# Kernel optimization log

Measured on AMD Instinct MI355X. Metric: run time of the kernel, lower is better.

## Reference

```python
import jax, jax.numpy as jnp
import numpy as np

K_MASK = -2.3819763e38  # gemma masking constant


def apply_rope(inputs, positions, head_dim):
    # inputs: [B, T, N, H], positions: [B, T]
    half = head_dim // 2
    fraction = 2.0 * jnp.arange(half, dtype=jnp.float32) / head_dim
    timescale = 10000.0 ** fraction                      # [half]
    sinusoid = positions[..., None].astype(jnp.float32) / timescale  # [B, T, half]
    sin = jnp.sin(sinusoid)[:, :, None, :]               # [B, T, 1, half]
    cos = jnp.cos(sinusoid)[:, :, None, :]
    first, second = jnp.split(inputs, 2, axis=-1)
    out = jnp.concatenate([first * cos - second * sin,
                           second * cos + first * sin], axis=-1)
    return out.astype(inputs.dtype)


def setup_inputs() -> dict:
    key = jax.random.key(0)
    k0, k1, k2, k3 = jax.random.split(key, 4)
    B, T, D, N, H = 4, 1024, 2048, 16, 128
    x = jax.random.normal(k0, (B, T, D), dtype=jnp.float32)
    wq = jax.random.normal(k1, (N, D, H), dtype=jnp.float32) * 0.02
    wkv = jax.random.normal(k2, (2, 1, D, H), dtype=jnp.float32) * 0.02  # MQA: 1 kv head
    wo = jax.random.normal(k3, (N, H, D), dtype=jnp.float32) * 0.02
    segment_pos = jnp.broadcast_to(jnp.arange(T, dtype=jnp.int32), (B, T))
    attn_mask = jnp.broadcast_to(jnp.tril(jnp.ones((T, T), dtype=bool)), (B, T, T))
    return {"x": x, "wq": wq, "wkv": wkv, "wo": wo,
            "segment_pos": segment_pos, "attn_mask": attn_mask}


def reference(x, wq, wkv, wo, segment_pos, attn_mask):
    N, _, H = wq.shape
    # projections
    q = jnp.einsum('BTD,NDH->BTNH', x, wq)          # [B,T,N,H]
    kv = jnp.einsum('BSD,CKDH->CBSKH', x, wkv)      # [2,B,S,1,H]
    k, v = kv[0], kv[1]
    # RoPE + scaling
    q = apply_rope(q, segment_pos, H) * (H ** -0.5)
    k = apply_rope(k, segment_pos, H)
    # MQA head repeat: 1 kv head -> N heads
    k = jnp.repeat(k, N, axis=-2)                   # [B,S,N,H]
    v = jnp.repeat(v, N, axis=-2)
    # attention with manual masked softmax
    logits = jnp.einsum('BTNH,BSNH->BTNS', q, k)
    padded = jnp.where(attn_mask[:, :, None, :], logits, K_MASK)
    probs = jax.nn.softmax(padded, axis=-1).astype(k.dtype)
    encoded = jnp.einsum('BTNS,BSNH->BTNH', probs, v)
    return jnp.einsum('BTNH,NHD->BTD', encoded, wo)
```

## Files before the change

### kernel.cpp

```cpp
#include <hip/hip_runtime.h>
#include <cstdint>
#include <cstddef>

typedef unsigned short u16;
typedef __attribute__((ext_vector_type(8))) short bf16x8;
typedef __attribute__((ext_vector_type(4))) float f32x4;
typedef __attribute__((ext_vector_type(16))) float f32x16;
typedef __attribute__((ext_vector_type(4))) uint32_t u32x4;

#define B_ 4
#define T_ 1024
#define D_ 2048
#define N_ 16
#define H_ 128
#define BT_ (B_ * T_)
#define KMASK (-2.3819763e38f)

__device__ __forceinline__ u16 f2bf(float f) {
  uint32_t u = __builtin_bit_cast(uint32_t, f);
  u += 0x7FFFu + ((u >> 16) & 1u);
  return (u16)(u >> 16);
}
__device__ __forceinline__ float bf2f(uint32_t u) {
  return __builtin_bit_cast(float, u << 16);
}

__device__ __forceinline__ float xhalf_max(float x) {
  return fmaxf(x, __shfl_xor(x, 32, 64));
}
__device__ __forceinline__ float xhalf_add(float x) {
  return x + __shfl_xor(x, 32, 64);
}

__device__ __forceinline__ void gload16(const void* g, void* l) {
  __builtin_amdgcn_global_load_lds((const __attribute__((address_space(1))) void*)g,
                                   (__attribute__((address_space(3))) void*)l, 16, 0, 0);
}

__global__ __launch_bounds__(256) void convert_x_kernel(const float* __restrict__ x,
                                                        u16* __restrict__ xb) {
  int i = (blockIdx.x * 256 + threadIdx.x) * 8;
  float4 v0 = *(const float4*)(x + i);
  float4 v1 = *(const float4*)(x + i + 4);
  uint4 o;
  o.x = (uint32_t)f2bf(v0.x) | ((uint32_t)f2bf(v0.y) << 16);
  o.y = (uint32_t)f2bf(v0.z) | ((uint32_t)f2bf(v0.w) << 16);
  o.z = (uint32_t)f2bf(v1.x) | ((uint32_t)f2bf(v1.y) << 16);
  o.w = (uint32_t)f2bf(v1.z) | ((uint32_t)f2bf(v1.w) << 16);
  *(uint4*)(xb + i) = o;
}

__global__ __launch_bounds__(256) void transpose_kernel(const float* __restrict__ src,
                                                        u16* __restrict__ dst, int R, int C) {
  __shared__ float tile[32][33];
  const int z = blockIdx.z;
  const float* s = src + (size_t)z * R * C;
  u16* d = dst + (size_t)z * R * C;
  const int tx = threadIdx.x, ty = threadIdx.y;
  const int r0 = blockIdx.y * 32, c0 = blockIdx.x * 32;
#pragma unroll
  for (int i = 0; i < 4; ++i)
    tile[ty + i * 8][tx] = s[(size_t)(r0 + ty + i * 8) * C + (c0 + tx)];
  __syncthreads();
#pragma unroll
  for (int i = 0; i < 4; ++i)
    d[(size_t)(c0 + ty + i * 8) * R + (r0 + tx)] = f2bf(tile[tx][ty + i * 8]);
}

__global__ __launch_bounds__(256) void rope_table_kernel(float* __restrict__ costab,
                                                         float* __restrict__ sintab) {
  int idx = blockIdx.x * 256 + threadIdx.x;
  int p = idx >> 6, i = idx & 63;
  float ts = powf(10000.0f, (float)i * (1.0f / 64.0f));
  float ang = (float)p / ts;
  costab[idx] = cosf(ang);
  sintab[idx] = sinf(ang);
}

__global__ __launch_bounds__(256) void proj_gemm_kernel(
    const u16* __restrict__ xb, const u16* __restrict__ wqT, const u16* __restrict__ wkvT,
    u16* __restrict__ qraw, u16* __restrict__ kraw, u16* __restrict__ vT) {
  __shared__ alignas(16) u16 a_lds[128 * 64];
  __shared__ alignas(16) u16 b_lds[128 * 64];
  const int bid = blockIdx.x;
  const int newbid = (bid & 7) * 72 + (bid >> 3);
  const int y = newbid >> 5;
  const int m0 = (newbid & 31) * 128;
  const u16* Bt = (y < N_) ? (wqT + (size_t)y * H_ * D_) : (wkvT + (size_t)(y - N_) * H_ * D_);
  const int tid = threadIdx.x;
  const int w = tid >> 6, lane = tid & 63;
  const int g = lane >> 4, li = lane & 15;
  const int mrow = (w >> 1) * 64, wc = (w & 1) * 64;
  f32x4 acc[4][4];
#pragma unroll
  for (int i = 0; i < 4; ++i)
#pragma unroll
    for (int j = 0; j < 4; ++j) acc[i][j] = (f32x4){0.f, 0.f, 0.f, 0.f};

  for (int k0 = 0; k0 < D_; k0 += 64) {
    __syncthreads();
#pragma unroll
    for (int it = 0; it < 4; ++it) {
      int chunk = it * 256 + tid;
      int row = chunk >> 3, cu = chunk & 7;
      gload16(xb + (size_t)(m0 + row) * D_ + k0 + ((cu ^ (row & 7)) << 3), &a_lds[chunk * 8]);
    }
#pragma unroll
    for (int it = 0; it < 4; ++it) {
      int chunk = it * 256 + tid;
      int row = chunk >> 3, cu = chunk & 7;
      gload16(Bt + (size_t)row * D_ + k0 + ((cu ^ (row & 7)) << 3), &b_lds[chunk * 8]);
    }
    __syncthreads();
#pragma unroll
    for (int c2 = 0; c2 < 2; ++c2) {
      bf16x8 af[4], bfr[4];
#pragma unroll
      for (int i = 0; i < 4; ++i) {
        int row = mrow + i * 16 + li;
        af[i] = *(const bf16x8*)((const char*)a_lds +
                                 row * 128 + ((c2 * 64 + g * 16) ^ ((row & 7) << 4)));
      }
#pragma unroll
      for (int j = 0; j < 4; ++j) {
        int row = wc + j * 16 + li;
        bfr[j] = *(const bf16x8*)((const char*)b_lds +
                                  row * 128 + ((c2 * 64 + g * 16) ^ ((row & 7) << 4)));
      }
#pragma unroll
      for (int i = 0; i < 4; ++i)
#pragma unroll
        for (int j = 0; j < 4; ++j)
          acc[i][j] = __builtin_amdgcn_mfma_f32_16x16x32_bf16(af[i], bfr[j], acc[i][j], 0, 0, 0);
    }
  }

  const int b = m0 >> 10;
  if (y == N_ + 1) {
    const int tbase0 = (m0 & 1023) + mrow;
#pragma unroll
    for (int i = 0; i < 4; ++i) {
      int tbase = tbase0 + i * 16 + g * 4;
#pragma unroll
      for (int j = 0; j < 4; ++j) {
        int h = wc + j * 16 + li;
        ushort4 pk;
        pk.x = f2bf(acc[i][j][0]);
        pk.y = f2bf(acc[i][j][1]);
        pk.z = f2bf(acc[i][j][2]);
        pk.w = f2bf(acc[i][j][3]);
        *(ushort4*)(vT + ((size_t)(b * H_ + h)) * T_ + tbase) = pk;
      }
    }
  } else {
    size_t rowbase = (y < N_) ? ((size_t)(b * N_ + y) * T_ + (m0 & 1023)) : (size_t)m0;
    u16* dst0 = (y < N_) ? qraw : kraw;
#pragma unroll
    for (int i = 0; i < 4; ++i)
#pragma unroll
      for (int r = 0; r < 4; ++r) {
        int trow = mrow + i * 16 + g * 4 + r;
        u16* dst = dst0 + (rowbase + trow) * H_;
#pragma unroll
        for (int j = 0; j < 4; ++j) dst[wc + j * 16 + li] = f2bf(acc[i][j][r]);
      }
  }
}

__global__ __launch_bounds__(256) void rope_apply_k_kernel(
    const u16* __restrict__ kraw, const int* __restrict__ segment_pos,
    const float* __restrict__ costab, const float* __restrict__ sintab,
    u16* __restrict__ kb) {
  const int rid = blockIdx.x * 8 + (threadIdx.x >> 5);
  const int j = threadIdx.x & 31;
  const u16* src = kraw + (size_t)rid * H_;
  u16* dst = kb + (size_t)rid * H_;
  int p = segment_pos[rid];
  p = p < 0 ? 0 : (p > 1023 ? 1023 : p);
  uint32_t ua = *(const uint32_t*)(src + 2 * j);
  uint32_t ub = *(const uint32_t*)(src + 64 + 2 * j);
  float2 cv = *(const float2*)(costab + p * 64 + 2 * j);
  float2 sv = *(const float2*)(sintab + p * 64 + 2 * j);
  float f1a = bf2f(ua & 0xffffu), f1b = bf2f(ua >> 16);
  float f2a = bf2f(ub & 0xffffu), f2b = bf2f(ub >> 16);
  *(uint32_t*)(dst + 2 * j) =
      (uint32_t)f2bf(f1a * cv.x - f2a * sv.x) | ((uint32_t)f2bf(f1b * cv.y - f2b * sv.y) << 16);
  *(uint32_t*)(dst + 64 + 2 * j) =
      (uint32_t)f2bf(f2a * cv.x + f1a * sv.x) | ((uint32_t)f2bf(f2b * cv.y + f1b * sv.y) << 16);
}

__global__ __launch_bounds__(128) void attn_kernel(
    const u16* __restrict__ qraw, const u16* __restrict__ kb, const u16* __restrict__ vT,
    const int* __restrict__ segment_pos, const float* __restrict__ costab,
    const float* __restrict__ sintab, u16* __restrict__ enc) {
  __shared__ alignas(16) u16 k_lds[2][64 * 128];
  __shared__ alignas(16) u16 v_lds[128 * 64];
  const int bx = blockIdx.x;
  const int qt = 15 - (bx >> 6);
  const int bn = bx & 63;
  const int b = bn >> 4, n = bn & 15;
  const int tid = threadIdx.x, w = tid >> 6, lane = tid & 63;
  const int l31 = lane & 31, hi = lane >> 5;
  const int t = qt * 64 + w * 32 + l31;

  bf16x8 qf[8];
  {
    const u16* qrow = qraw + ((size_t)(b * N_ + n) * T_ + t) * H_;
#pragma unroll
    for (int kc = 0; kc < 8; ++kc) qf[kc] = *(const bf16x8*)(qrow + kc * 16 + hi * 8);
    int p = segment_pos[b * T_ + t];
    p = p < 0 ? 0 : (p > 1023 ? 1023 : p);
    const float scale = 0.12751743342f;
#pragma unroll
    for (int kc = 0; kc < 4; ++kc) {
      const float* cp = costab + p * 64 + kc * 16 + hi * 8;
      const float* sp = sintab + p * 64 + kc * 16 + hi * 8;
#pragma unroll
      for (int e = 0; e < 8; ++e) {
        float cv = cp[e], sv = sp[e];
        float f1 = bf2f((u16)qf[kc][e]);
        float f2 = bf2f((u16)qf[kc + 4][e]);
        qf[kc][e] = (short)f2bf((f1 * cv - f2 * sv) * scale);
        qf[kc + 4][e] = (short)f2bf((f2 * cv + f1 * sv) * scale);
      }
    }
  }

  f32x16 o[4];
#pragma unroll
  for (int hc = 0; hc < 4; ++hc)
#pragma unroll
    for (int r = 0; r < 16; ++r) o[hc][r] = 0.f;
  float m_ = -3e38f, lsum = 0.f;

  auto stageK = [&](int buf, int s0) {
#pragma unroll
    for (int it = 0; it < 8; ++it) {
      int chunk = it * 128 + tid;
      int row = chunk >> 4, cu = chunk & 15;
      gload16(kb + ((size_t)b * T_ + s0 + row) * H_ + ((cu ^ (row & 7)) << 3),
              &k_lds[buf][chunk * 8]);
    }
  };
  auto stageV = [&](int s0) {
#pragma unroll
    for (int it = 0; it < 8; ++it) {
      int chunk = it * 128 + tid;
      int row = chunk >> 3, cu = chunk & 7;
      gload16(vT + ((size_t)(b * H_ + row)) * T_ + s0 + ((cu ^ (row & 7)) << 3),
              &v_lds[chunk * 8]);
    }
  };

  const int nst = qt + 1;
  stageK(0, 0);
  int cur = 0;
  for (int st = 0; st < nst; ++st) {
    const int s0 = st * 64;
    const bool pre = (st + 1 < nst);
    stageV(s0);
    if (pre) stageK(cur ^ 1, s0 + 64);
    if (pre) asm volatile("s_waitcnt vmcnt(16)" ::: "memory");
    else     asm volatile("s_waitcnt vmcnt(8)" ::: "memory");
    __builtin_amdgcn_sched_barrier(0);
    __builtin_amdgcn_s_barrier();

    f32x16 sacc[2];
#pragma unroll
    for (int sub = 0; sub < 2; ++sub)
#pragma unroll
      for (int r = 0; r < 16; ++r) sacc[sub][r] = 0.f;
    __builtin_amdgcn_s_setprio(1);
#pragma unroll
    for (int kc = 0; kc < 8; ++kc)
#pragma unroll
      for (int sub = 0; sub < 2; ++sub) {
        int srow = sub * 32 + l31;
        bf16x8 kf = *(const bf16x8*)((const char*)&k_lds[cur][0] + srow * 256 +
                                     ((kc * 32 + hi * 16) ^ ((srow & 7) << 4)));
        sacc[sub] = __builtin_amdgcn_mfma_f32_32x32x16_bf16(kf, qf[kc], sacc[sub], 0, 0, 0);
      }
    __builtin_amdgcn_s_setprio(0);

    if (st == qt) {
#pragma unroll
      for (int sub = 0; sub < 2; ++sub)
#pragma unroll
        for (int r = 0; r < 16; ++r) {
          int s = s0 + sub * 32 + (r & 3) + 8 * (r >> 2) + 4 * hi;
          if (s > t) sacc[sub][r] = KMASK;
        }
    }

    float mx = -3e38f;
#pragma unroll
    for (int sub = 0; sub < 2; ++sub)
#pragma unroll
      for (int r = 0; r < 16; ++r) mx = fmaxf(mx, sacc[sub][r]);
    mx = xhalf_max(mx);
    if (__any(mx - m_ > 11.5f)) {
      float mn = fmaxf(m_, mx);
      float alpha = exp2f(m_ - mn);
      m_ = mn;
      lsum *= alpha;
#pragma unroll
      for (int hc = 0; hc < 4; ++hc)
#pragma unroll
        for (int r = 0; r < 16; ++r) o[hc][r] *= alpha;
    }
    float ps = 0.f;
#pragma unroll
    for (int sub = 0; sub < 2; ++sub)
#pragma unroll
      for (int r = 0; r < 16; ++r) {
        float pv = exp2f(sacc[sub][r] - m_);
        sacc[sub][r] = pv;
        ps += pv;
      }
    lsum += xhalf_add(ps);

    if (pre) asm volatile("s_waitcnt vmcnt(8)" ::: "memory");
    else     asm volatile("s_waitcnt vmcnt(0)" ::: "memory");
    __builtin_amdgcn_sched_barrier(0);
    __builtin_amdgcn_s_barrier();

    __builtin_amdgcn_s_setprio(1);
#pragma unroll
    for (int sc = 0; sc < 4; ++sc) {
      const int sub = sc >> 1, rb = (sc & 1) * 8;
      uint32_t a0, a1, b0, b1;
      asm("v_cvt_pk_bf16_f32 %0, %1, %2" : "=v"(a0) : "v"(sacc[sub][rb + 0]), "v"(sacc[sub][rb + 1]));
      asm("v_cvt_pk_bf16_f32 %0, %1, %2" : "=v"(a1) : "v"(sacc[sub][rb + 2]), "v"(sacc[sub][rb + 3]));
      asm("v_cvt_pk_bf16_f32 %0, %1, %2" : "=v"(b0) : "v"(sacc[sub][rb + 4]), "v"(sacc[sub][rb + 5]));
      asm("v_cvt_pk_bf16_f32 %0, %1, %2" : "=v"(b1) : "v"(sacc[sub][rb + 6]), "v"(sacc[sub][rb + 7]));
      uint32_t pa0 = (uint32_t)__shfl_xor((int)a0, 32, 64);
      uint32_t pa1 = (uint32_t)__shfl_xor((int)a1, 32, 64);
      uint32_t pb0 = (uint32_t)__shfl_xor((int)b0, 32, 64);
      uint32_t pb1 = (uint32_t)__shfl_xor((int)b1, 32, 64);
      uint32_t d0 = hi ? pb0 : a0;
      uint32_t d1 = hi ? pb1 : a1;
      uint32_t d2 = hi ? b0 : pa0;
      uint32_t d3 = hi ? b1 : pa1;
      u32x4 pdv = (u32x4){d0, d1, d2, d3};
      bf16x8 pf = __builtin_bit_cast(bf16x8, pdv);
#pragma unroll
      for (int hc = 0; hc < 4; ++hc) {
        int hrow = hc * 32 + l31;
        bf16x8 vf = *(const bf16x8*)((const char*)v_lds + hrow * 128 +
                                     ((sc * 32 + hi * 16) ^ ((hrow & 7) << 4)));
        o[hc] = __builtin_amdgcn_mfma_f32_32x32x16_bf16(vf, pf, o[hc], 0, 0, 0);
      }
    }
    __builtin_amdgcn_s_setprio(0);
    __builtin_amdgcn_s_barrier();
    cur ^= 1;
  }

  float inv = 1.0f / lsum;
  u16* dst = enc + ((size_t)(b * T_ + t)) * (N_ * H_) + n * H_;
#pragma unroll
  for (int hc = 0; hc < 4; ++hc)
#pragma unroll
    for (int rq = 0; rq < 4; ++rq) {
      ushort4 pk;
      pk.x = f2bf(o[hc][rq * 4 + 0] * inv);
      pk.y = f2bf(o[hc][rq * 4 + 1] * inv);
      pk.z = f2bf(o[hc][rq * 4 + 2] * inv);
      pk.w = f2bf(o[hc][rq * 4 + 3] * inv);
      *(ushort4*)(dst + hc * 32 + rq * 8 + hi * 4) = pk;
    }
}

__global__ __launch_bounds__(256) void out_gemm_kernel(const u16* __restrict__ enc,
                                                       const u16* __restrict__ woT,
                                                       float* __restrict__ out) {
  __shared__ alignas(16) u16 a_lds[128 * 64];
  __shared__ alignas(16) u16 b_lds[128 * 64];
  const int bid = blockIdx.x;
  const int newbid = (bid & 7) * 64 + (bid >> 3);
  const int m0 = (newbid & 31) * 128;
  const int n0 = (newbid >> 5) * 128;
  const int tid = threadIdx.x, w = tid >> 6, lane = tid & 63;
  const int g = lane >> 4, li = lane & 15;
  const int mrow = (w >> 1) * 64, wc = (w & 1) * 64;
  f32x4 acc[4][4];
#pragma unroll
  for (int i = 0; i < 4; ++i)
#pragma unroll
    for (int j = 0; j < 4; ++j) acc[i][j] = (f32x4){0.f, 0.f, 0.f, 0.f};

  for (int k0 = 0; k0 < D_; k0 += 64) {
    __syncthreads();
#pragma unroll
    for (int it = 0; it < 4; ++it) {
      int chunk = it * 256 + tid;
      int row = chunk >> 3, cu = chunk & 7;
      gload16(enc + (size_t)(m0 + row) * D_ + k0 + ((cu ^ (row & 7)) << 3), &a_lds[chunk * 8]);
    }
#pragma unroll
    for (int it = 0; it < 4; ++it) {
      int chunk = it * 256 + tid;
      int row = chunk >> 3, cu = chunk & 7;
      gload16(woT + (size_t)(n0 + row) * D_ + k0 + ((cu ^ (row & 7)) << 3), &b_lds[chunk * 8]);
    }
    __syncthreads();
#pragma unroll
    for (int c2 = 0; c2 < 2; ++c2) {
      bf16x8 af[4], bfr[4];
#pragma unroll
      for (int i = 0; i < 4; ++i) {
        int row = mrow + i * 16 + li;
        af[i] = *(const bf16x8*)((const char*)a_lds +
                                 row * 128 + ((c2 * 64 + g * 16) ^ ((row & 7) << 4)));
      }
#pragma unroll
      for (int j = 0; j < 4; ++j) {
        int row = wc + j * 16 + li;
        bfr[j] = *(const bf16x8*)((const char*)b_lds +
                                  row * 128 + ((c2 * 64 + g * 16) ^ ((row & 7) << 4)));
      }
#pragma unroll
      for (int i = 0; i < 4; ++i)
#pragma unroll
        for (int j = 0; j < 4; ++j)
          acc[i][j] = __builtin_amdgcn_mfma_f32_16x16x32_bf16(af[i], bfr[j], acc[i][j], 0, 0, 0);
    }
  }
#pragma unroll
  for (int i = 0; i < 4; ++i)
#pragma unroll
    for (int r = 0; r < 4; ++r) {
      int bt = m0 + mrow + i * 16 + g * 4 + r;
      float* dst = out + (size_t)bt * D_ + n0 + wc;
#pragma unroll
      for (int j = 0; j < 4; ++j) dst[j * 16 + li] = acc[i][j][r];
    }
}

extern "C" void kernel_launch(void* const* d_in, const int* in_sizes, int n_in,
                              void* d_out, int out_size, void* d_ws, size_t ws_size,
                              hipStream_t stream) {
  const float* x = (const float*)d_in[0];
  const float* wq = (const float*)d_in[1];
  const float* wkv = (const float*)d_in[2];
  const float* wo = (const float*)d_in[3];
  const int* segment_pos = (const int*)d_in[4];
  float* out = (float*)d_out;

  char* ws = (char*)d_ws;
  size_t off = 0;
  auto alloc = [&](size_t bytes) -> void* {
    void* p = ws + off;
    off += (bytes + 255) & ~(size_t)255;
    return p;
  };
  u16* xb   = (u16*)alloc((size_t)BT_ * D_ * 2);
  u16* wqT  = (u16*)alloc((size_t)N_ * H_ * D_ * 2);
  u16* wkvT = (u16*)alloc((size_t)2 * H_ * D_ * 2);
  u16* woT  = (u16*)alloc((size_t)D_ * N_ * H_ * 2);
  u16* qraw = (u16*)alloc((size_t)B_ * N_ * T_ * H_ * 2);
  u16* kb   = (u16*)alloc((size_t)B_ * T_ * H_ * 2);
  u16* kraw = (u16*)alloc((size_t)B_ * T_ * H_ * 2);
  u16* vT   = (u16*)alloc((size_t)B_ * H_ * T_ * 2);
  u16* enc  = (u16*)alloc((size_t)BT_ * N_ * H_ * 2);
  float* costab = (float*)alloc(1024 * 64 * 4);
  float* sintab = (float*)alloc(1024 * 64 * 4);

  convert_x_kernel<<<BT_ * D_ / 8 / 256, 256, 0, stream>>>(x, xb);
  dim3 tb(32, 8);
  transpose_kernel<<<dim3(H_ / 32, D_ / 32, N_), tb, 0, stream>>>(wq, wqT, D_, H_);
  transpose_kernel<<<dim3(H_ / 32, D_ / 32, 2), tb, 0, stream>>>(wkv, wkvT, D_, H_);
  transpose_kernel<<<dim3(D_ / 32, D_ / 32, 1), tb, 0, stream>>>(wo, woT, N_ * H_, D_);
  rope_table_kernel<<<256, 256, 0, stream>>>(costab, sintab);
  proj_gemm_kernel<<<576, 256, 0, stream>>>(xb, wqT, wkvT, qraw, kraw, vT);
  rope_apply_k_kernel<<<BT_ / 8, 256, 0, stream>>>(kraw, segment_pos, costab, sintab, kb);
  attn_kernel<<<1024, 128, 0, stream>>>(qraw, kb, vT, segment_pos, costab, sintab, enc);
  out_gemm_kernel<<<512, 256, 0, stream>>>(enc, woT, out);
}
```

Measured before the change: 180.2 us.

## Shrink attention blocks to single-wave 32-row tiles and drop block barriers

The attention kernel now runs one 64-lane wave per block over 32 query rows, with 32-key KV tiles, and launches twice as many blocks. With a single wave, the s_barrier calls are removed, and an lgkmcnt wait keeps LDS reads finished before the next staging overwrites the buffers. Smaller tiles give finer causal granularity, which means less wasted masked work on the diagonal, and more blocks for occupancy. The cost is that K/V tiles are no longer shared across two waves, so each K/V byte is loaded from global into LDS twice as often, and each step does fewer MFMAs per load.

```diff
diff --git a/kernel.cpp b/kernel.cpp
--- a/kernel.cpp
+++ b/kernel.cpp
@@ -189,19 +189,19 @@
       (uint32_t)f2bf(f2a * cv.x + f1a * sv.x) | ((uint32_t)f2bf(f2b * cv.y + f1b * sv.y) << 16);
 }
 
-__global__ __launch_bounds__(128) void attn_kernel(
+__global__ __launch_bounds__(64) void attn_kernel(
     const u16* __restrict__ qraw, const u16* __restrict__ kb, const u16* __restrict__ vT,
     const int* __restrict__ segment_pos, const float* __restrict__ costab,
     const float* __restrict__ sintab, u16* __restrict__ enc) {
-  __shared__ alignas(16) u16 k_lds[2][64 * 128];
-  __shared__ alignas(16) u16 v_lds[128 * 64];
+  __shared__ alignas(16) u16 k_lds[2][32 * 128];
+  __shared__ alignas(16) u16 v_lds[128 * 32];
   const int bx = blockIdx.x;
-  const int qt = 15 - (bx >> 6);
+  const int qt = 31 - (bx >> 6);
   const int bn = bx & 63;
   const int b = bn >> 4, n = bn & 15;
-  const int tid = threadIdx.x, w = tid >> 6, lane = tid & 63;
+  const int lane = threadIdx.x & 63;
   const int l31 = lane & 31, hi = lane >> 5;
-  const int t = qt * 64 + w * 32 + l31;
+  const int t = qt * 32 + l31;
 
   bf16x8 qf[8];
   {
@@ -236,7 +236,7 @@
   auto stageK = [&](int buf, int s0) {
 #pragma unroll
     for (int it = 0; it < 8; ++it) {
-      int chunk = it * 128 + tid;
+      int chunk = it * 64 + lane;
       int row = chunk >> 4, cu = chunk & 15;
       gload16(kb + ((size_t)b * T_ + s0 + row) * H_ + ((cu ^ (row & 7)) << 3),
               &k_lds[buf][chunk * 8]);
@@ -245,9 +245,9 @@
   auto stageV = [&](int s0) {
 #pragma unroll
     for (int it = 0; it < 8; ++it) {
-      int chunk = it * 128 + tid;
-      int row = chunk >> 3, cu = chunk & 7;
-      gload16(vT + ((size_t)(b * H_ + row)) * T_ + s0 + ((cu ^ (row & 7)) << 3),
+      int chunk = it * 64 + lane;
+      int row = chunk >> 2, cu = chunk & 3;
+      gload16(vT + ((size_t)(b * H_ + row)) * T_ + s0 + ((cu ^ (row & 3)) << 3),
               &v_lds[chunk * 8]);
     }
   };
@@ -256,47 +256,40 @@
   stageK(0, 0);
   int cur = 0;
   for (int st = 0; st < nst; ++st) {
-    const int s0 = st * 64;
+    const int s0 = st * 32;
     const bool pre = (st + 1 < nst);
+    asm volatile("s_waitcnt lgkmcnt(0)" ::: "memory");
+    __builtin_amdgcn_sched_barrier(0);
     stageV(s0);
-    if (pre) stageK(cur ^ 1, s0 + 64);
+    if (pre) stageK(cur ^ 1, s0 + 32);
     if (pre) asm volatile("s_waitcnt vmcnt(16)" ::: "memory");
     else     asm volatile("s_waitcnt vmcnt(8)" ::: "memory");
     __builtin_amdgcn_sched_barrier(0);
-    __builtin_amdgcn_s_barrier();
-
-    f32x16 sacc[2];
-#pragma unroll
-    for (int sub = 0; sub < 2; ++sub)
-#pragma unroll
-      for (int r = 0; r < 16; ++r) sacc[sub][r] = 0.f;
+
+    f32x16 sacc;
+#pragma unroll
+    for (int r = 0; r < 16; ++r) sacc[r] = 0.f;
     __builtin_amdgcn_s_setprio(1);
 #pragma unroll
-    for (int kc = 0; kc < 8; ++kc)
-#pragma unroll
-      for (int sub = 0; sub < 2; ++sub) {
-        int srow = sub * 32 + l31;
-        bf16x8 kf = *(const bf16x8*)((const char*)&k_lds[cur][0] + srow * 256 +
-                                     ((kc * 32 + hi * 16) ^ ((srow & 7) << 4)));
-        sacc[sub] = __builtin_amdgcn_mfma_f32_32x32x16_bf16(kf, qf[kc], sacc[sub], 0, 0, 0);
-      }
+    for (int kc = 0; kc < 8; ++kc) {
+      int srow = l31;
+      bf16x8 kf = *(const bf16x8*)((const char*)&k_lds[cur][0] + srow * 256 +
+                                   ((kc * 32 + hi * 16) ^ ((srow & 7) << 4)));
+      sacc = __builtin_amdgcn_mfma_f32_32x32x16_bf16(kf, qf[kc], sacc, 0, 0, 0);
+    }
     __builtin_amdgcn_s_setprio(0);
 
     if (st == qt) {
 #pragma unroll
-      for (int sub = 0; sub < 2; ++sub)
-#pragma unroll
-        for (int r = 0; r < 16; ++r) {
-          int s = s0 + sub * 32 + (r & 3) + 8 * (r >> 2) + 4 * hi;
-          if (s > t) sacc[sub][r] = KMASK;
-        }
+      for (int r = 0; r < 16; ++r) {
+        int s = s0 + (r & 3) + 8 * (r >> 2) + 4 * hi;
+        if (s > t) sacc[r] = KMASK;
+      }
     }
 
     float mx = -3e38f;
 #pragma unroll
-    for (int sub = 0; sub < 2; ++sub)
-#pragma unroll
-      for (int r = 0; r < 16; ++r) mx = fmaxf(mx, sacc[sub][r]);
+    for (int r = 0; r < 16; ++r) mx = fmaxf(mx, sacc[r]);
     mx = xhalf_max(mx);
     if (__any(mx - m_ > 11.5f)) {
       float mn = fmaxf(m_, mx);
@@ -310,29 +303,26 @@
     }
     float ps = 0.f;
 #pragma unroll
-    for (int sub = 0; sub < 2; ++sub)
-#pragma unroll
-      for (int r = 0; r < 16; ++r) {
-        float pv = exp2f(sacc[sub][r] - m_);
-        sacc[sub][r] = pv;
-        ps += pv;
-      }
+    for (int r = 0; r < 16; ++r) {
+      float pv = exp2f(sacc[r] - m_);
+      sacc[r] = pv;
+      ps += pv;
+    }
     lsum += xhalf_add(ps);
 
     if (pre) asm volatile("s_waitcnt vmcnt(8)" ::: "memory");
     else     asm volatile("s_waitcnt vmcnt(0)" ::: "memory");
     __builtin_amdgcn_sched_barrier(0);
-    __builtin_amdgcn_s_barrier();
 
     __builtin_amdgcn_s_setprio(1);
 #pragma unroll
-    for (int sc = 0; sc < 4; ++sc) {
-      const int sub = sc >> 1, rb = (sc & 1) * 8;
+    for (int sc = 0; sc < 2; ++sc) {
+      const int rb = sc * 8;
       uint32_t a0, a1, b0, b1;
-      asm("v_cvt_pk_bf16_f32 %0, %1, %2" : "=v"(a0) : "v"(sacc[sub][rb + 0]), "v"(sacc[sub][rb + 1]));
-      asm("v_cvt_pk_bf16_f32 %0, %1, %2" : "=v"(a1) : "v"(sacc[sub][rb + 2]), "v"(sacc[sub][rb + 3]));
-      asm("v_cvt_pk_bf16_f32 %0, %1, %2" : "=v"(b0) : "v"(sacc[sub][rb + 4]), "v"(sacc[sub][rb + 5]));
-      asm("v_cvt_pk_bf16_f32 %0, %1, %2" : "=v"(b1) : "v"(sacc[sub][rb + 6]), "v"(sacc[sub][rb + 7]));
+      asm("v_cvt_pk_bf16_f32 %0, %1, %2" : "=v"(a0) : "v"(sacc[rb + 0]), "v"(sacc[rb + 1]));
+      asm("v_cvt_pk_bf16_f32 %0, %1, %2" : "=v"(a1) : "v"(sacc[rb + 2]), "v"(sacc[rb + 3]));
+      asm("v_cvt_pk_bf16_f32 %0, %1, %2" : "=v"(b0) : "v"(sacc[rb + 4]), "v"(sacc[rb + 5]));
+      asm("v_cvt_pk_bf16_f32 %0, %1, %2" : "=v"(b1) : "v"(sacc[rb + 6]), "v"(sacc[rb + 7]));
       uint32_t pa0 = (uint32_t)__shfl_xor((int)a0, 32, 64);
       uint32_t pa1 = (uint32_t)__shfl_xor((int)a1, 32, 64);
       uint32_t pb0 = (uint32_t)__shfl_xor((int)b0, 32, 64);
@@ -346,13 +336,12 @@
 #pragma unroll
       for (int hc = 0; hc < 4; ++hc) {
         int hrow = hc * 32 + l31;
-        bf16x8 vf = *(const bf16x8*)((const char*)v_lds + hrow * 128 +
-                                     ((sc * 32 + hi * 16) ^ ((hrow & 7) << 4)));
+        bf16x8 vf = *(const bf16x8*)((const char*)v_lds + hrow * 64 +
+                                     ((sc * 32 + hi * 16) ^ ((hrow & 3) << 4)));
         o[hc] = __builtin_amdgcn_mfma_f32_32x32x16_bf16(vf, pf, o[hc], 0, 0, 0);
       }
     }
     __builtin_amdgcn_s_setprio(0);
-    __builtin_amdgcn_s_barrier();
     cur ^= 1;
   }
 
@@ -474,6 +463,6 @@
   rope_table_kernel<<<256, 256, 0, stream>>>(costab, sintab);
   proj_gemm_kernel<<<576, 256, 0, stream>>>(xb, wqT, wkvT, qraw, kraw, vT);
   rope_apply_k_kernel<<<BT_ / 8, 256, 0, stream>>>(kraw, segment_pos, costab, sintab, kb);
-  attn_kernel<<<1024, 128, 0, stream>>>(qraw, kb, vT, segment_pos, costab, sintab, enc);
+  attn_kernel<<<2048, 64, 0, stream>>>(qraw, kb, vT, segment_pos, costab, sintab, enc);
   out_gemm_kernel<<<512, 256, 0, stream>>>(enc, woT, out);
 }
```

Result: slower. 189.7 us (+5.3%).
